# Kernel tuning notes

Measured on AMD Instinct MI355X. Metric: run time of the kernel, lower is better.

Reference implementation:

```python
import jax, jax.numpy as jnp
import numpy as np

DIM = 512
HIDDEN = 2048
D_M = 256
R = 64
GEN_HIDDEN = D_M * 2  # hidden_mul=2
ALPHA_MEM = 1.0


def setup_inputs() -> dict:
    key = jax.random.key(0)
    ks = jax.random.split(key, 12)
    B, T = 2, 512
    inp = {
        'x': jax.random.normal(ks[0], (B, T, DIM), jnp.float32),
        'm_tok': jax.random.normal(ks[1], (B, T, D_M), jnp.float32),
        # base SwiGLU params
        'W1': jax.random.normal(ks[2], (HIDDEN, DIM), jnp.float32) * (1.0 / np.sqrt(DIM)),
        'W2': jax.random.normal(ks[3], (HIDDEN, DIM), jnp.float32) * (1.0 / np.sqrt(DIM)),
        'W3': jax.random.normal(ks[4], (DIM, HIDDEN), jnp.float32) * (1.0 / np.sqrt(HIDDEN)),
        'b1': jnp.zeros((HIDDEN,), jnp.float32),
        'b2': jnp.zeros((HIDDEN,), jnp.float32),
        'b3': jnp.zeros((DIM,), jnp.float32),
        # hypernetwork (FFNMemGenerator): d_m -> gen_hidden -> 3*r*dim
        'gen_w1': jax.random.normal(ks[5], (GEN_HIDDEN, D_M), jnp.float32) * (1.0 / np.sqrt(D_M)),
        'gen_b1': jnp.zeros((GEN_HIDDEN,), jnp.float32),
        'gen_w2': jax.random.normal(ks[6], (3 * R * DIM, GEN_HIDDEN), jnp.float32) * (0.02 / np.sqrt(GEN_HIDDEN)),
        'gen_b2': jnp.zeros((3 * R * DIM,), jnp.float32),
        'mem_gate': jnp.zeros((), jnp.float32),
    }
    return inp


def reference(x, m_tok, W1, W2, W3, b1, b2, b3, gen_w1, gen_b1, gen_w2, gen_b2, mem_gate):
    B, T, _ = x.shape
    # base SwiGLU FFN
    x1 = jnp.einsum('od,btd->bto', W1, x) + b1  # [B,T,hidden]
    x2 = jnp.einsum('od,btd->bto', W2, x) + b2
    h_base = jax.nn.silu(x1) * x2
    y_base = jnp.einsum('do,bto->btd', W3, h_base) + b3  # [B,T,dim]

    # hypernetwork-generated per-token low-rank weights
    hg = jax.nn.silu(jnp.einsum('hd,btd->bth', gen_w1, m_tok) + gen_b1)
    w = jnp.einsum('oh,bth->bto', gen_w2, hg) + gen_b2  # [B,T,3*r*dim]
    W1_m = w[..., : R * DIM].reshape(B, T, R, DIM)
    W2_m = w[..., R * DIM : 2 * R * DIM].reshape(B, T, R, DIM)
    W3_m = w[..., 2 * R * DIM :].reshape(B, T, DIM, R)

    # per-token batched matvecs (memory path)
    u1 = jnp.einsum('btrd,btd->btr', W1_m, x)
    u2 = jnp.einsum('btrd,btd->btr', W2_m, x)
    h_mem = jax.nn.silu(u1) * u2
    y_mem = jnp.einsum('btdr,btr->btd', W3_m, h_mem)

    g = jax.nn.sigmoid(mem_gate)
    return y_base + g * ALPHA_MEM * y_mem
```

## Files before the change

### kernel.cpp

```cpp
#include <hip/hip_runtime.h>
#include <cstdint>
#include <cstddef>

#define TOK   1024
#define DIMX  512
#define HID   2048
#define DM    256
#define GENH  512
#define RR    64
#define O3BASE 65536

typedef __bf16 bf16x8 __attribute__((ext_vector_type(8)));
typedef float  f32x4  __attribute__((ext_vector_type(4)));

#define SB0 __builtin_amdgcn_sched_barrier(0)

__device__ __forceinline__ unsigned short f2bf(float f) {
  union { float f; uint32_t u; } v; v.f = f;
  return (unsigned short)((v.u + 0x7fffu + ((v.u >> 16) & 1u)) >> 16);
}
__device__ __forceinline__ float bf2f(unsigned short h) {
  union { uint32_t u; float f; } v; v.u = (uint32_t)h << 16;
  return v.f;
}
__device__ __forceinline__ float silu_f(float x) { return x / (1.f + __expf(-x)); }

__device__ __forceinline__ void async_copy16(const void* g, void* l) {
  __builtin_amdgcn_global_load_lds(
      (const __attribute__((address_space(1))) void*)g,
      (__attribute__((address_space(3))) void*)l, 16, 0, 0);
}

__device__ __forceinline__ void cast8(const float* __restrict__ src,
                                      unsigned short* __restrict__ dst, size_t i) {
  float4 v0 = *(const float4*)(src + i);
  float4 v1 = *(const float4*)(src + i + 4);
  ushort4 h0, h1;
  h0.x = f2bf(v0.x); h0.y = f2bf(v0.y); h0.z = f2bf(v0.z); h0.w = f2bf(v0.w);
  h1.x = f2bf(v1.x); h1.y = f2bf(v1.y); h1.z = f2bf(v1.z); h1.w = f2bf(v1.w);
  *(ushort4*)(dst + i)     = h0;
  *(ushort4*)(dst + i + 4) = h1;
}

template<int ROWS>
__device__ __forceinline__ void stage_tile(
    const unsigned short* __restrict__ base, size_t row0, int stride, int kofs,
    unsigned short* Ls, int tid) {
  constexpr int IT = ROWS / 32;
  const int wave = tid >> 6, lane = tid & 63;
#pragma unroll
  for (int j = 0; j < IT; ++j) {
    int s   = wave * (IT * 64) + j * 64 + lane;
    int row = s >> 3;
    int kc  = (s & 7) ^ (row & 7);
    const unsigned short* g = base + (row0 + (size_t)row) * (size_t)stride + kofs + kc * 8;
    async_copy16(g, (char*)Ls + wave * (IT * 1024) + j * 1024);
  }
}

template<int KLEN, int MF>
__device__ __forceinline__ void mfma_tile_nt(
    const unsigned short* __restrict__ Abf, size_t a_row0, int astride,
    const unsigned short* __restrict__ Bbf, size_t b_row0, int bstride, int k0,
    unsigned short* As, unsigned short* Bs, f32x4 (&acc)[MF][4], int tid) {
  const int lane = tid & 63;
  const int wave = tid >> 6;
  const int m0 = (wave >> 1) * (MF * 16), n0 = (wave & 1) * 64;

  for (int kk = 0; kk < KLEN; kk += 64) {
    stage_tile<MF * 32>(Abf, a_row0, astride, k0 + kk, As, tid);
    stage_tile<128>(Bbf, b_row0, bstride, k0 + kk, Bs, tid);
    __syncthreads();
#pragma unroll
    for (int ks = 0; ks < 2; ++ks) {
      int cbase = ks * 4 + (lane >> 4);
      int koff  = (cbase ^ (lane & 7)) * 8;
      bf16x8 a[MF], b[4];
#pragma unroll
      for (int mf = 0; mf < MF; ++mf)
        a[mf] = *(const bf16x8*)(As + (m0 + mf * 16 + (lane & 15)) * 64 + koff);
#pragma unroll
      for (int nf = 0; nf < 4; ++nf)
        b[nf] = *(const bf16x8*)(Bs + (n0 + nf * 16 + (lane & 15)) * 64 + koff);
#pragma unroll
      for (int mf = 0; mf < MF; ++mf)
#pragma unroll
        for (int nf = 0; nf < 4; ++nf)
          acc[mf][nf] = __builtin_amdgcn_mfma_f32_16x16x32_bf16(
              a[mf], b[nf], acc[mf][nf], 0, 0, 0);
    }
    __syncthreads();
  }
}

template<int MF>
__device__ __forceinline__ void zero_accN(f32x4 (&acc)[MF][4]) {
#pragma unroll
  for (int i = 0; i < MF; ++i)
#pragma unroll
    for (int j = 0; j < 4; ++j) {
      f32x4 z = {0.f, 0.f, 0.f, 0.f};
      acc[i][j] = z;
    }
}

__device__ __forceinline__ void mfma_256_async(
    const unsigned short* __restrict__ Abf, size_t a_row0,
    const unsigned short* __restrict__ Bbf, size_t b_row0,
    unsigned short* As, unsigned short* Bs, f32x4 (&acc)[8][4]) {
  const int tid = threadIdx.x, lane = tid & 63, wave = tid >> 6;
  const int wr = wave >> 2, wc = wave & 3;
  const int m0 = wr * 128, n0 = wc * 64;
  const int l15 = lane & 15;
  constexpr int ABUF = 256 * 64, BBUF = 256 * 64;

  const unsigned short *gA[4], *gB[4];
  const int sbase = wave * 256 + lane;
#pragma unroll
  for (int jj = 0; jj < 4; ++jj) {
    int s = sbase + jj * 64;
    int row = s >> 3;
    int kc  = (s & 7) ^ (row & 7);
    gA[jj] = Abf + (a_row0 + (size_t)row) * GENH + kc * 8;
    gB[jj] = Bbf + (b_row0 + (size_t)row) * GENH + kc * 8;
  }

  bf16x8 bfr[4], afr[4];

  auto stage = [&](int k0, unsigned short* Ad, unsigned short* Bd) {
#pragma unroll
    for (int jj = 0; jj < 4; ++jj)
      async_copy16(gA[jj] + k0, (char*)Ad + (wave * 4 + jj) * 1024);
#pragma unroll
    for (int jj = 0; jj < 4; ++jj)
      async_copy16(gB[jj] + k0, (char*)Bd + (wave * 4 + jj) * 1024);
  };
  auto rdB = [&](const unsigned short* Bb, int ks) {
    int koff = (((ks << 2) + (lane >> 4)) ^ (lane & 7)) << 3;
#pragma unroll
    for (int nf = 0; nf < 4; ++nf)
      bfr[nf] = *(const bf16x8*)(Bb + (n0 + nf * 16 + l15) * 64 + koff);
  };
  auto rdA = [&](const unsigned short* Ab, int ks, int mh) {
    int koff = (((ks << 2) + (lane >> 4)) ^ (lane & 7)) << 3;
#pragma unroll
    for (int i = 0; i < 4; ++i)
      afr[i] = *(const bf16x8*)(Ab + (m0 + (mh * 4 + i) * 16 + l15) * 64 + koff);
  };
  auto mfma16 = [&](int mh) {
    __builtin_amdgcn_s_setprio(1);
#pragma unroll
    for (int i = 0; i < 4; ++i)
#pragma unroll
      for (int nf = 0; nf < 4; ++nf)
        acc[mh * 4 + i][nf] = __builtin_amdgcn_mfma_f32_16x16x32_bf16(
            afr[i], bfr[nf], acc[mh * 4 + i][nf], 0, 0, 0);
    __builtin_amdgcn_s_setprio(0);
  };

  stage(0, As, Bs);
  asm volatile("s_waitcnt vmcnt(0)" ::: "memory");
  __syncthreads();

  int cur = 0;
#pragma unroll 1
  for (int t = 0; t < 8; ++t) {
    unsigned short* Ac = As + cur * ABUF;
    unsigned short* Bc = Bs + cur * BBUF;
    if (t < 7)
      stage((t + 1) * 64, As + (cur ^ 1) * ABUF, Bs + (cur ^ 1) * BBUF);
    SB0;
    rdB(Bc, 0); rdA(Ac, 0, 0);
    mfma16(0);
    SB0;
    rdA(Ac, 0, 1);
    mfma16(1);
    SB0;
    rdB(Bc, 1); rdA(Ac, 1, 0);
    mfma16(0);
    SB0;
    rdA(Ac, 1, 1);
    mfma16(1);
    SB0;
    asm volatile("s_waitcnt vmcnt(0)" ::: "memory");
    __syncthreads();
    cur ^= 1;
  }
}

__global__ __launch_bounds__(256) void prep_kernel(
    const float* __restrict__ x, const float* __restrict__ m_tok,
    const float* __restrict__ gen_w1, const float* __restrict__ gen_b1,
    const float* __restrict__ W1, const float* __restrict__ W2,
    const float* __restrict__ W3, const float* __restrict__ gen_w2,
    unsigned short* __restrict__ xb, unsigned short* __restrict__ hgb,
    unsigned short* __restrict__ W1b, unsigned short* __restrict__ W2b,
    unsigned short* __restrict__ W3b, unsigned short* __restrict__ w2b) {
  const int tid = threadIdx.x;
  if (blockIdx.x >= 256) {
    const size_t cb = blockIdx.x - 256;
#pragma unroll
    for (int k = 0; k < 8; ++k) {
      size_t i = ((size_t)k * 524288 + cb * 256 + tid) * 8;
      cast8(gen_w2, w2b, i);
    }
    return;
  }
  __shared__ float mt[4 * DM];
  const size_t t0 = (size_t)blockIdx.x * 4;
#pragma unroll
  for (int k = 0; k < 4; ++k) mt[k * 256 + tid] = m_tok[t0 * DM + k * 256 + tid];
#pragma unroll
  for (int k = 0; k < 8; ++k) {
    size_t idx = t0 * DIMX + k * 256 + tid;
    xb[idx] = f2bf(x[idx]);
  }
  {
    size_t base = ((size_t)blockIdx.x * 256 + tid) * 8;
#pragma unroll
    for (int it = 0; it < 2; ++it) {
      size_t idx = base + (size_t)it * 524288;
      cast8(W1, W1b, idx);
      cast8(W2, W2b, idx);
      cast8(W3, W3b, idx);
    }
  }
  __syncthreads();
#pragma unroll
  for (int hh = 0; hh < 2; ++hh) {
    int h = hh * 256 + tid;
    float a0, a1, a2, a3;
    a0 = a1 = a2 = a3 = gen_b1[h];
    const float* wr = gen_w1 + (size_t)h * DM;
    for (int d = 0; d < DM; d += 4) {
      float4 w = *(const float4*)(wr + d);
      a0 += w.x * mt[d]       + w.y * mt[d + 1]       + w.z * mt[d + 2]       + w.w * mt[d + 3];
      a1 += w.x * mt[256 + d] + w.y * mt[256 + d + 1] + w.z * mt[256 + d + 2] + w.w * mt[256 + d + 3];
      a2 += w.x * mt[512 + d] + w.y * mt[512 + d + 1] + w.z * mt[512 + d + 2] + w.w * mt[512 + d + 3];
      a3 += w.x * mt[768 + d] + w.y * mt[768 + d + 1] + w.z * mt[768 + d + 2] + w.w * mt[768 + d + 3];
    }
    hgb[(t0 + 0) * GENH + h] = f2bf(silu_f(a0));
    hgb[(t0 + 1) * GENH + h] = f2bf(silu_f(a1));
    hgb[(t0 + 2) * GENH + h] = f2bf(silu_f(a2));
    hgb[(t0 + 3) * GENH + h] = f2bf(silu_f(a3));
  }
}

__device__ __forceinline__ void ffn12_body(
    int bx, const unsigned short* __restrict__ xb, const unsigned short* __restrict__ W1b,
    const unsigned short* __restrict__ W2b, const float* __restrict__ pb1,
    const float* __restrict__ pb2, unsigned short* __restrict__ hb,
    unsigned short* As, unsigned short* B1s, unsigned short* B2s, int tid) {
  const int lane = tid & 63, wave = tid >> 6;
  const int ob = bx & 15, tb = bx >> 4;
  const size_t t0 = (size_t)tb * 32, o0 = (size_t)ob * 128;
  const int m0 = (wave >> 1) * 16, n0 = (wave & 1) * 64;

  f32x4 acc1[4], acc2[4];
#pragma unroll
  for (int j = 0; j < 4; ++j) {
    f32x4 z = {0.f, 0.f, 0.f, 0.f};
    acc1[j] = z; acc2[j] = z;
  }

  for (int kk = 0; kk < DIMX; kk += 64) {
    stage_tile<32>(xb, t0, DIMX, kk, As, tid);
    stage_tile<128>(W1b, o0, DIMX, kk, B1s, tid);
    stage_tile<128>(W2b, o0, DIMX, kk, B2s, tid);
    __syncthreads();
#pragma unroll
    for (int ks = 0; ks < 2; ++ks) {
      int cbase = ks * 4 + (lane >> 4);
      int koff  = (cbase ^ (lane & 7)) * 8;
      bf16x8 a, b1[4], b2[4];
      a = *(const bf16x8*)(As + (m0 + (lane & 15)) * 64 + koff);
#pragma unroll
      for (int nf = 0; nf < 4; ++nf) {
        b1[nf] = *(const bf16x8*)(B1s + (n0 + nf * 16 + (lane & 15)) * 64 + koff);
        b2[nf] = *(const bf16x8*)(B2s + (n0 + nf * 16 + (lane & 15)) * 64 + koff);
      }
#pragma unroll
      for (int nf = 0; nf < 4; ++nf) {
        acc1[nf] = __builtin_amdgcn_mfma_f32_16x16x32_bf16(a, b1[nf], acc1[nf], 0, 0, 0);
        acc2[nf] = __builtin_amdgcn_mfma_f32_16x16x32_bf16(a, b2[nf], acc2[nf], 0, 0, 0);
      }
    }
    __syncthreads();
  }

  const int q = lane >> 4;
  float b1v[4], b2v[4];
#pragma unroll
  for (int nf = 0; nf < 4; ++nf) {
    b1v[nf] = pb1[o0 + n0 + nf * 16 + (lane & 15)];
    b2v[nf] = pb2[o0 + n0 + nf * 16 + (lane & 15)];
  }
#pragma unroll
  for (int nf = 0; nf < 4; ++nf)
#pragma unroll
    for (int rg = 0; rg < 4; ++rg) {
      size_t trow = t0 + m0 + q * 4 + rg;
      size_t col  = o0 + n0 + nf * 16 + (lane & 15);
      float v1 = acc1[nf][rg] + b1v[nf];
      float v2 = acc2[nf][rg] + b2v[nf];
      hb[trow * HID + col] = f2bf(silu_f(v1) * v2);
    }
}

union SmemUV {
  struct { unsigned short As[2 * 256 * 64], Bs[2 * 256 * 64]; } ab;
  struct { unsigned short Xs[256 * 256]; } ep;
};

__device__ __forceinline__ void memuv_body(
    int bx, const unsigned short* __restrict__ hgb, const unsigned short* __restrict__ w2b,
    const float* __restrict__ gen_b2, const unsigned short* __restrict__ xb,
    float* __restrict__ up, SmemUV& sm) {
  const int s8 = bx & 7, w = bx >> 3;
  const int n = s8 * 32 + (w >> 2), m = w & 3;
  const size_t N0 = (size_t)n * 256, t0 = (size_t)m * 256;
  const int stripA = n << 1;
  const int j  = n >> 1;
  const int d0 = (stripA & 3) * 128;

  f32x4 acc[8][4];
  zero_accN<8>(acc);
  mfma_256_async(hgb, t0, w2b, N0, sm.ab.As, sm.ab.Bs, acc);

  const int tid = threadIdx.x, lane = tid & 63, wave = tid >> 6;
  const int wr = wave >> 2, wc = wave & 3;
#pragma unroll
  for (int i = 0; i < 16; ++i) {
    int qq = i * 512 + tid;
    int row = qq >> 5, c = qq & 31;
    const unsigned short* src = xb + (t0 + (size_t)row) * DIMX + d0 + c * 8;
    ushort4 v0 = *(const ushort4*)src;
    ushort4 v1 = *(const ushort4*)(src + 4);
    int cs = c ^ (((row >> 2) & 3) << 1);
    unsigned short* dst = sm.ep.Xs + row * 256 + cs * 8;
    *(ushort4*)dst = v0;
    *(ushort4*)(dst + 4) = v1;
  }
  __syncthreads();

  const int m0 = wr * 128, n0 = wc * 64;
  const int q = lane >> 4, l15 = lane & 15;
  float gbv[4];
#pragma unroll
  for (int i = 0; i < 4; ++i)
    gbv[i] = gen_b2[N0 + n0 + i * 16 + l15];

  const int p = ((stripA + (wc >> 1)) & 3) * 2 + (wc & 1);
  float* upd = up + (size_t)p * (128 * 1024) + (size_t)j * 1024 + t0;
#pragma unroll
  for (int mf = 0; mf < 8; ++mf) {
    f32x4 vals;
#pragma unroll
    for (int rg = 0; rg < 4; ++rg) {
      int trow = m0 + mf * 16 + q * 4 + rg;
      int swz  = ((trow >> 2) & 3) << 1;
      float val = 0.f;
#pragma unroll
      for (int nf = 0; nf < 4; ++nf) {
        int col = n0 + nf * 16 + l15;
        int gct = col >> 3;
        int idx = trow * 256 + ((gct ^ swz) << 3) + (col & 7);
        val += (acc[mf][nf][rg] + gbv[nf]) * bf2f(sm.ep.Xs[idx]);
      }
      val += __shfl_xor(val, 1);
      val += __shfl_xor(val, 2);
      val += __shfl_xor(val, 4);
      val += __shfl_xor(val, 8);
      vals[rg] = val;
    }
    if (l15 == 0)
      *(f32x4*)(upd + m0 + mf * 16 + q * 4) = vals;
  }
}

union SmemK2 {
  SmemUV m;
  struct { unsigned short As[2][32 * 64], B1s[2][128 * 64], B2s[2][128 * 64]; } f;
};

__global__ __launch_bounds__(512, 2) void k2_kernel(
    const unsigned short* __restrict__ xb, const unsigned short* __restrict__ W1b,
    const unsigned short* __restrict__ W2b, const float* __restrict__ b1,
    const float* __restrict__ b2, unsigned short* __restrict__ hb,
    const unsigned short* __restrict__ hgb, const float* __restrict__ gw2,
    unsigned short* __restrict__ w2b, const float* __restrict__ gen_b2,
    float* __restrict__ up) {
  __shared__ SmemK2 sm;
  const int bx = blockIdx.x;
  if (bx < 1024) {
    memuv_body(bx, hgb, w2b, gen_b2, xb, up, sm.m);
  } else if (bx < 1280) {
    const int sub = threadIdx.x >> 8, tloc = threadIdx.x & 255;
    const int vb = (bx - 1024) * 2 + sub;
    ffn12_body(vb, xb, W1b, W2b, b1, b2, hb,
               sm.f.As[sub], sm.f.B1s[sub], sm.f.B2s[sub], tloc);
  } else {
    const size_t cb = bx - 1280, tid = threadIdx.x;
#pragma unroll
    for (int k = 0; k < 16; ++k) {
      size_t i = 33554432 + ((size_t)k * 131072 + cb * 512 + tid) * 8;
      cast8(gw2, w2b, i);
    }
  }
}

__device__ __forceinline__ void gemm3p_body(
    int bx, const unsigned short* __restrict__ hb, const unsigned short* __restrict__ W3b,
    float* __restrict__ yp, unsigned short* As, unsigned short* Bs) {
  const int slice = bx >> 6, r6 = bx & 63;
  const int ob = r6 & 3, tb = r6 >> 2;
  const size_t o0 = (size_t)ob * 128, t0 = (size_t)tb * 64;
  const int k0 = slice * 512;
  const int tid = threadIdx.x;
  f32x4 acc[2][4];
  zero_accN<2>(acc);
  mfma_tile_nt<512, 2>(hb, t0, HID, W3b, o0, HID, k0, As, Bs, acc, tid);

  const int lane = tid & 63, wave = tid >> 6;
  const int m0 = (wave >> 1) * 32, n0 = (wave & 1) * 64;
  float* out = yp + (size_t)slice * (TOK * DIMX);
#pragma unroll
  for (int nf = 0; nf < 4; ++nf) {
    int nn = n0 + nf * 16 + (lane & 15);
#pragma unroll
    for (int mf = 0; mf < 2; ++mf) {
      int mb = m0 + mf * 16 + ((lane >> 4) << 2);
#pragma unroll
      for (int rg = 0; rg < 4; ++rg)
        out[(t0 + mb + rg) * DIMX + o0 + nn] = acc[mf][nf][rg];
    }
  }
}

__device__ __forceinline__ void hmem_body(int bx, const float* __restrict__ up,
                                          float* __restrict__ hm) {
  int i = bx * 256 + threadIdx.x;
  int t = i & 1023, r = i >> 10;
  float u1 = 0.f, u2 = 0.f;
#pragma unroll
  for (int p = 0; p < 8; ++p) {
    u1 += up[(size_t)p * (128 * 1024) + (size_t)r * 1024 + t];
    u2 += up[(size_t)p * (128 * 1024) + (size_t)(64 + r) * 1024 + t];
  }
  hm[(size_t)t * RR + r] = silu_f(u1) * u2;
}

union SmemK3 {
  struct { unsigned short As[64 * 64], Bs[128 * 64]; } g;
};

__global__ __launch_bounds__(256) void k3_kernel(
    const unsigned short* __restrict__ hb, const unsigned short* __restrict__ W3b,
    float* __restrict__ yp, const float* __restrict__ up, float* __restrict__ hm) {
  __shared__ SmemK3 sm;
  const int bx = blockIdx.x;
  if (bx < 256)
    gemm3p_body(bx, hb, W3b, yp, sm.g.As, sm.g.Bs);
  else
    hmem_body(bx - 256, up, hm);
}

union SmemY {
  struct { unsigned short As[2 * 256 * 64], Bs[2 * 256 * 64]; } ab;
  struct { float Hs[256 * 64]; } ep;
};

__global__ __launch_bounds__(512, 2) void memy_kernel(
    const unsigned short* __restrict__ hgb, const unsigned short* __restrict__ w2b,
    const float* __restrict__ gen_b2, const float* __restrict__ hmem,
    const float* __restrict__ yp, const float* __restrict__ b3,
    const float* __restrict__ mem_gate, float* __restrict__ y) {
  __shared__ SmemY sm;
  const int bx = blockIdx.x;
  const int s8 = bx & 7, w = bx >> 3;
  const int n = s8 * 16 + (w >> 2), m = w & 3;
  const size_t N0 = (size_t)n * 256;
  const size_t brow0 = (size_t)O3BASE + N0;
  const size_t t0 = (size_t)m * 256;

  f32x4 acc[8][4];
  zero_accN<8>(acc);
  mfma_256_async(hgb, t0, w2b, brow0, sm.ab.As, sm.ab.Bs, acc);

  const int tid = threadIdx.x, lane = tid & 63, wave = tid >> 6;
  const int wr = wave >> 2, wc = wave & 3;
#pragma unroll
  for (int i = 0; i < 8; ++i) {
    int qq = i * 512 + tid;
    int row = qq >> 4, c = qq & 15;
    float4 vv = *(const float4*)(hmem + (t0 + (size_t)row) * RR + c * 4);
    int cs = c ^ (((row >> 2) & 3) << 2);
    *(float4*)(sm.ep.Hs + row * 64 + cs * 4) = vv;
  }
  __syncthreads();

  const int m0 = wr * 128, n0 = wc * 64;
  const int q = lane >> 4, l15 = lane & 15;
  const float g = 1.f / (1.f + __expf(-mem_gate[0]));
  float gbv[4];
#pragma unroll
  for (int i = 0; i < 4; ++i)
    gbv[i] = gen_b2[brow0 + n0 + i * 16 + l15];

  const int d = (int)(N0 >> 6) + wc;
  const float b3v = b3[d];
#pragma unroll
  for (int mf = 0; mf < 8; ++mf)
#pragma unroll
    for (int rg = 0; rg < 4; ++rg) {
      int trow = m0 + mf * 16 + q * 4 + rg;
      int swz  = ((trow >> 2) & 3) << 2;
      float val = 0.f;
#pragma unroll
      for (int nf = 0; nf < 4; ++nf) {
        int r = nf * 16 + l15;
        int idx = trow * 64 + (((r >> 2) ^ swz) << 2) + (r & 3);
        val += (acc[mf][nf][rg] + gbv[nf]) * sm.ep.Hs[idx];
      }
      val += __shfl_xor(val, 1);
      val += __shfl_xor(val, 2);
      val += __shfl_xor(val, 4);
      val += __shfl_xor(val, 8);
      if (l15 == 0) {
        size_t gi = (t0 + trow) * DIMX + d;
        float base = b3v + yp[gi]
                   + yp[(size_t)1 * (TOK * DIMX) + gi]
                   + yp[(size_t)2 * (TOK * DIMX) + gi]
                   + yp[(size_t)3 * (TOK * DIMX) + gi];
        y[gi] = base + g * val;
      }
    }
}

extern "C" void kernel_launch(void* const* d_in, const int* in_sizes, int n_in,
                              void* d_out, int out_size, void* d_ws, size_t ws_size,
                              hipStream_t stream) {
  const float* x        = (const float*)d_in[0];
  const float* m_tok    = (const float*)d_in[1];
  const float* W1       = (const float*)d_in[2];
  const float* W2       = (const float*)d_in[3];
  const float* W3       = (const float*)d_in[4];
  const float* b1       = (const float*)d_in[5];
  const float* b2       = (const float*)d_in[6];
  const float* b3       = (const float*)d_in[7];
  const float* gen_w1   = (const float*)d_in[8];
  const float* gen_b1   = (const float*)d_in[9];
  const float* gen_w2   = (const float*)d_in[10];
  const float* gen_b2   = (const float*)d_in[11];
  const float* mem_gate = (const float*)d_in[12];
  float* y = (float*)d_out;

  char* ws = (char*)d_ws;
#define KB(v) ((size_t)(v) << 10)
  unsigned short* xb  = (unsigned short*)(ws);
  unsigned short* hgb = (unsigned short*)(ws + KB(1024));
  unsigned short* hb  = (unsigned short*)(ws + KB(2048));
  float* up  = (float*)(ws + KB(6144));
  float* hm  = (float*)(ws + KB(10240));
  float* yp  = (float*)(ws + KB(10752));
  unsigned short* W1b = (unsigned short*)(ws + KB(21248));
  unsigned short* W2b = (unsigned short*)(ws + KB(23296));
  unsigned short* W3b = (unsigned short*)(ws + KB(25344));
  unsigned short* w2b = (unsigned short*)(ws + KB(27392));
#undef KB

  prep_kernel<<<256 + 2048, 256, 0, stream>>>(x, m_tok, gen_w1, gen_b1,
                                              W1, W2, W3, gen_w2,
                                              xb, hgb, W1b, W2b, W3b, w2b);
  k2_kernel<<<1024 + 256 + 256, 512, 0, stream>>>(xb, W1b, W2b, b1, b2, hb,
                                                  hgb, gen_w2, w2b, gen_b2, up);
  k3_kernel<<<256 + 256, 256, 0, stream>>>(hb, W3b, yp, up, hm);
  memy_kernel<<<512, 512, 0, stream>>>(hgb, w2b, gen_b2, hm, yp, b3,
                                       mem_gate, y);
}
```

Before: 479.8 us.

## Transpose x and permute h_mem layout for vectorized epilogue reads; simplify MFMA loop

Prep now also writes a transposed bf16 copy of x, so the memuv epilogue can stage it column-major in LDS and read four consecutive tokens per lane as one vector load instead of scalar gathers. h_mem is stored with a permuted r index, so memy's epilogue reads one float4 per row without the XOR swizzle. The hand-scheduled MFMA pipeline with sched_barriers and setprio is replaced by a plain unrolled loop, leaving instruction scheduling to the compiler. The costs are an extra strided scatter write of x in prep and the loss of explicit scheduling control.

```diff
diff --git a/kernel.cpp b/kernel.cpp
--- a/kernel.cpp
+++ b/kernel.cpp
@@ -12,8 +12,6 @@
 
 typedef __bf16 bf16x8 __attribute__((ext_vector_type(8)));
 typedef float  f32x4  __attribute__((ext_vector_type(4)));
-
-#define SB0 __builtin_amdgcn_sched_barrier(0)
 
 __device__ __forceinline__ unsigned short f2bf(float f) {
   union { float f; uint32_t u; } v; v.f = f;
@@ -125,8 +123,6 @@
     gB[jj] = Bbf + (b_row0 + (size_t)row) * GENH + kc * 8;
   }
 
-  bf16x8 bfr[4], afr[4];
-
   auto stage = [&](int k0, unsigned short* Ad, unsigned short* Bd) {
 #pragma unroll
     for (int jj = 0; jj < 4; ++jj)
@@ -135,28 +131,6 @@
     for (int jj = 0; jj < 4; ++jj)
       async_copy16(gB[jj] + k0, (char*)Bd + (wave * 4 + jj) * 1024);
   };
-  auto rdB = [&](const unsigned short* Bb, int ks) {
-    int koff = (((ks << 2) + (lane >> 4)) ^ (lane & 7)) << 3;
-#pragma unroll
-    for (int nf = 0; nf < 4; ++nf)
-      bfr[nf] = *(const bf16x8*)(Bb + (n0 + nf * 16 + l15) * 64 + koff);
-  };
-  auto rdA = [&](const unsigned short* Ab, int ks, int mh) {
-    int koff = (((ks << 2) + (lane >> 4)) ^ (lane & 7)) << 3;
-#pragma unroll
-    for (int i = 0; i < 4; ++i)
-      afr[i] = *(const bf16x8*)(Ab + (m0 + (mh * 4 + i) * 16 + l15) * 64 + koff);
-  };
-  auto mfma16 = [&](int mh) {
-    __builtin_amdgcn_s_setprio(1);
-#pragma unroll
-    for (int i = 0; i < 4; ++i)
-#pragma unroll
-      for (int nf = 0; nf < 4; ++nf)
-        acc[mh * 4 + i][nf] = __builtin_amdgcn_mfma_f32_16x16x32_bf16(
-            afr[i], bfr[nf], acc[mh * 4 + i][nf], 0, 0, 0);
-    __builtin_amdgcn_s_setprio(0);
-  };
 
   stage(0, As, Bs);
   asm volatile("s_waitcnt vmcnt(0)" ::: "memory");
@@ -165,23 +139,31 @@
   int cur = 0;
 #pragma unroll 1
   for (int t = 0; t < 8; ++t) {
-    unsigned short* Ac = As + cur * ABUF;
-    unsigned short* Bc = Bs + cur * BBUF;
+    const unsigned short* Ac = As + cur * ABUF;
+    const unsigned short* Bc = Bs + cur * BBUF;
     if (t < 7)
       stage((t + 1) * 64, As + (cur ^ 1) * ABUF, Bs + (cur ^ 1) * BBUF);
-    SB0;
-    rdB(Bc, 0); rdA(Ac, 0, 0);
-    mfma16(0);
-    SB0;
-    rdA(Ac, 0, 1);
-    mfma16(1);
-    SB0;
-    rdB(Bc, 1); rdA(Ac, 1, 0);
-    mfma16(0);
-    SB0;
-    rdA(Ac, 1, 1);
-    mfma16(1);
-    SB0;
+#pragma unroll
+    for (int ks = 0; ks < 2; ++ks) {
+      int koff = (((ks << 2) + (lane >> 4)) ^ (lane & 7)) << 3;
+      bf16x8 bfr[4];
+#pragma unroll
+      for (int nf = 0; nf < 4; ++nf)
+        bfr[nf] = *(const bf16x8*)(Bc + (n0 + nf * 16 + l15) * 64 + koff);
+#pragma unroll
+      for (int mh = 0; mh < 2; ++mh) {
+        bf16x8 afr[4];
+#pragma unroll
+        for (int i = 0; i < 4; ++i)
+          afr[i] = *(const bf16x8*)(Ac + (m0 + (mh * 4 + i) * 16 + l15) * 64 + koff);
+#pragma unroll
+        for (int i = 0; i < 4; ++i)
+#pragma unroll
+          for (int nf = 0; nf < 4; ++nf)
+            acc[mh * 4 + i][nf] = __builtin_amdgcn_mfma_f32_16x16x32_bf16(
+                afr[i], bfr[nf], acc[mh * 4 + i][nf], 0, 0, 0);
+      }
+    }
     asm volatile("s_waitcnt vmcnt(0)" ::: "memory");
     __syncthreads();
     cur ^= 1;
@@ -193,7 +175,8 @@
     const float* __restrict__ gen_w1, const float* __restrict__ gen_b1,
     const float* __restrict__ W1, const float* __restrict__ W2,
     const float* __restrict__ W3, const float* __restrict__ gen_w2,
-    unsigned short* __restrict__ xb, unsigned short* __restrict__ hgb,
+    unsigned short* __restrict__ xb, unsigned short* __restrict__ xbT,
+    unsigned short* __restrict__ hgb,
     unsigned short* __restrict__ W1b, unsigned short* __restrict__ W2b,
     unsigned short* __restrict__ W3b, unsigned short* __restrict__ w2b) {
   const int tid = threadIdx.x;
@@ -212,8 +195,11 @@
   for (int k = 0; k < 4; ++k) mt[k * 256 + tid] = m_tok[t0 * DM + k * 256 + tid];
 #pragma unroll
   for (int k = 0; k < 8; ++k) {
-    size_t idx = t0 * DIMX + k * 256 + tid;
-    xb[idx] = f2bf(x[idx]);
+    int e = k * 256 + tid;
+    size_t idx = t0 * DIMX + e;
+    unsigned short b = f2bf(x[idx]);
+    xb[idx] = b;
+    xbT[(size_t)(e & 511) * TOK + t0 + (e >> 9)] = b;
   }
   {
     size_t base = ((size_t)blockIdx.x * 256 + tid) * 8;
@@ -314,7 +300,7 @@
 
 __device__ __forceinline__ void memuv_body(
     int bx, const unsigned short* __restrict__ hgb, const unsigned short* __restrict__ w2b,
-    const float* __restrict__ gen_b2, const unsigned short* __restrict__ xb,
+    const float* __restrict__ gen_b2, const unsigned short* __restrict__ xbT,
     float* __restrict__ up, SmemUV& sm) {
   const int s8 = bx & 7, w = bx >> 3;
   const int n = s8 * 32 + (w >> 2), m = w & 3;
@@ -333,10 +319,10 @@
   for (int i = 0; i < 16; ++i) {
     int qq = i * 512 + tid;
     int row = qq >> 5, c = qq & 31;
-    const unsigned short* src = xb + (t0 + (size_t)row) * DIMX + d0 + c * 8;
+    const unsigned short* src = xbT + (size_t)(d0 + row) * TOK + t0 + c * 8;
     ushort4 v0 = *(const ushort4*)src;
     ushort4 v1 = *(const ushort4*)(src + 4);
-    int cs = c ^ (((row >> 2) & 3) << 1);
+    int cs = c ^ (row & 7);
     unsigned short* dst = sm.ep.Xs + row * 256 + cs * 8;
     *(ushort4*)dst = v0;
     *(ushort4*)(dst + 4) = v1;
@@ -354,19 +340,24 @@
   float* upd = up + (size_t)p * (128 * 1024) + (size_t)j * 1024 + t0;
 #pragma unroll
   for (int mf = 0; mf < 8; ++mf) {
+    const int tbb = (m0 + mf * 16 + q * 4) * 2;
+    const int chunk = (tbb >> 4) ^ (l15 & 7);
+    float xr[4][4];
+#pragma unroll
+    for (int nf = 0; nf < 4; ++nf) {
+      int col = n0 + nf * 16 + l15;
+      ushort4 xv = *(const ushort4*)((const char*)sm.ep.Xs
+                     + (size_t)col * 512 + (chunk << 4) + (tbb & 15));
+      xr[nf][0] = bf2f(xv.x); xr[nf][1] = bf2f(xv.y);
+      xr[nf][2] = bf2f(xv.z); xr[nf][3] = bf2f(xv.w);
+    }
     f32x4 vals;
 #pragma unroll
     for (int rg = 0; rg < 4; ++rg) {
-      int trow = m0 + mf * 16 + q * 4 + rg;
-      int swz  = ((trow >> 2) & 3) << 1;
       float val = 0.f;
 #pragma unroll
-      for (int nf = 0; nf < 4; ++nf) {
-        int col = n0 + nf * 16 + l15;
-        int gct = col >> 3;
-        int idx = trow * 256 + ((gct ^ swz) << 3) + (col & 7);
-        val += (acc[mf][nf][rg] + gbv[nf]) * bf2f(sm.ep.Xs[idx]);
-      }
+      for (int nf = 0; nf < 4; ++nf)
+        val += (acc[mf][nf][rg] + gbv[nf]) * xr[nf][rg];
       val += __shfl_xor(val, 1);
       val += __shfl_xor(val, 2);
       val += __shfl_xor(val, 4);
@@ -384,7 +375,8 @@
 };
 
 __global__ __launch_bounds__(512, 2) void k2_kernel(
-    const unsigned short* __restrict__ xb, const unsigned short* __restrict__ W1b,
+    const unsigned short* __restrict__ xb, const unsigned short* __restrict__ xbT,
+    const unsigned short* __restrict__ W1b,
     const unsigned short* __restrict__ W2b, const float* __restrict__ b1,
     const float* __restrict__ b2, unsigned short* __restrict__ hb,
     const unsigned short* __restrict__ hgb, const float* __restrict__ gw2,
@@ -393,7 +385,7 @@
   __shared__ SmemK2 sm;
   const int bx = blockIdx.x;
   if (bx < 1024) {
-    memuv_body(bx, hgb, w2b, gen_b2, xb, up, sm.m);
+    memuv_body(bx, hgb, w2b, gen_b2, xbT, up, sm.m);
   } else if (bx < 1280) {
     const int sub = threadIdx.x >> 8, tloc = threadIdx.x & 255;
     const int vb = (bx - 1024) * 2 + sub;
@@ -447,7 +439,7 @@
     u1 += up[(size_t)p * (128 * 1024) + (size_t)r * 1024 + t];
     u2 += up[(size_t)p * (128 * 1024) + (size_t)(64 + r) * 1024 + t];
   }
-  hm[(size_t)t * RR + r] = silu_f(u1) * u2;
+  hm[(size_t)t * RR + ((r & 15) * 4 + (r >> 4))] = silu_f(u1) * u2;
 }
 
 union SmemK3 {
@@ -493,9 +485,8 @@
   for (int i = 0; i < 8; ++i) {
     int qq = i * 512 + tid;
     int row = qq >> 4, c = qq & 15;
-    float4 vv = *(const float4*)(hmem + (t0 + (size_t)row) * RR + c * 4);
-    int cs = c ^ (((row >> 2) & 3) << 2);
-    *(float4*)(sm.ep.Hs + row * 64 + cs * 4) = vv;
+    *(float4*)(sm.ep.Hs + row * 64 + c * 4) =
+        *(const float4*)(hmem + (t0 + (size_t)row) * RR + c * 4);
   }
   __syncthreads();
 
@@ -514,14 +505,11 @@
 #pragma unroll
     for (int rg = 0; rg < 4; ++rg) {
       int trow = m0 + mf * 16 + q * 4 + rg;
-      int swz  = ((trow >> 2) & 3) << 2;
-      float val = 0.f;
-#pragma unroll
-      for (int nf = 0; nf < 4; ++nf) {
-        int r = nf * 16 + l15;
-        int idx = trow * 64 + (((r >> 2) ^ swz) << 2) + (r & 3);
-        val += (acc[mf][nf][rg] + gbv[nf]) * sm.ep.Hs[idx];
-      }
+      f32x4 xv = *(const f32x4*)(sm.ep.Hs + trow * 64 + l15 * 4);
+      float val = (acc[mf][0][rg] + gbv[0]) * xv[0]
+                + (acc[mf][1][rg] + gbv[1]) * xv[1]
+                + (acc[mf][2][rg] + gbv[2]) * xv[2]
+                + (acc[mf][3][rg] + gbv[3]) * xv[3];
       val += __shfl_xor(val, 1);
       val += __shfl_xor(val, 2);
       val += __shfl_xor(val, 4);
@@ -567,12 +555,13 @@
   unsigned short* W2b = (unsigned short*)(ws + KB(23296));
   unsigned short* W3b = (unsigned short*)(ws + KB(25344));
   unsigned short* w2b = (unsigned short*)(ws + KB(27392));
+  unsigned short* xbT = (unsigned short*)(ws + KB(125696));
 #undef KB
 
   prep_kernel<<<256 + 2048, 256, 0, stream>>>(x, m_tok, gen_w1, gen_b1,
                                               W1, W2, W3, gen_w2,
-                                              xb, hgb, W1b, W2b, W3b, w2b);
-  k2_kernel<<<1024 + 256 + 256, 512, 0, stream>>>(xb, W1b, W2b, b1, b2, hb,
+                                              xb, xbT, hgb, W1b, W2b, W3b, w2b);
+  k2_kernel<<<1024 + 256 + 256, 512, 0, stream>>>(xb, xbT, W1b, W2b, b1, b2, hb,
                                                   hgb, gen_w2, w2b, gen_b2, up);
   k3_kernel<<<256 + 256, 256, 0, stream>>>(hb, W3b, yp, up, hm);
   memy_kernel<<<512, 512, 0, stream>>>(hgb, w2b, gen_b2, hm, yp, b3,
```

Result: no change. 480.4 us (+0.1%).
